# Kernel optimization log

Measured on AMD Instinct MI355X. Metric: run time of the kernel, lower is better.

The kernel has to match this reference:

```python
import jax, jax.numpy as jnp
import numpy as np

B, T, C, HS = 8, 2048, 1024, 64


def setup_inputs() -> dict:
    key = jax.random.key(0)
    ks = jax.random.split(key, 4)
    x = jax.random.normal(ks[0], (B, T, C), dtype=jnp.float32)
    Wq = jax.random.normal(ks[1], (C, HS), dtype=jnp.float32) * (C ** -0.5)
    Wk = jax.random.normal(ks[2], (C, HS), dtype=jnp.float32) * (C ** -0.5)
    Wv = jax.random.normal(ks[3], (C, HS), dtype=jnp.float32) * (C ** -0.5)
    mask = jnp.tril(jnp.ones((T, T), dtype=jnp.int32))  # causal mask
    return {"x": x, "mask": mask, "Wq": Wq, "Wk": Wk, "Wv": Wv}


def reference(x, mask, Wq, Wk, Wv):
    # x: [B,T,C]; bias-free projections to head_size
    q = jnp.einsum("btc,ch->bth", x, Wq)
    k = jnp.einsum("btc,ch->bth", x, Wk)
    v = jnp.einsum("btc,ch->bth", x, Wv)
    # NOTE: original scales by C**-0.5 (n_embd), not head_size**-0.5
    wei = jnp.einsum("bth,bsh->bts", q, k) * (x.shape[-1] ** -0.5)
    wei = jnp.where(mask[None, :, :] == 0, -jnp.inf, wei)
    wei = jax.nn.softmax(wei, axis=-1)
    # dropout is identity in eval / p=0
    out = jnp.einsum("bts,bsh->bth", wei, v)
    return out
```

## Files before the change

kernel.cpp:

```cpp
#include <hip/hip_runtime.h>
#include <hip/hip_bf16.h>


#define B_  8
#define T_  2048
#define C_  1024
#define HS_ 64
#define MROWS (B_ * T_)

typedef __attribute__((ext_vector_type(8))) short bf16x8;
typedef __attribute__((ext_vector_type(4))) float f32x4;
typedef __attribute__((ext_vector_type(4))) float float4v;

#define SCALE_LOG2 0.04508422037445829f

__device__ __forceinline__ short f2bs(float f) {
    __hip_bfloat16 h = __float2bfloat16(f);
    short s;
    __builtin_memcpy(&s, &h, 2);
    return s;
}

__global__ __launch_bounds__(256) void wt_kernel(
    const float* __restrict__ Wq,
    const float* __restrict__ Wk,
    const float* __restrict__ Wv,
    __hip_bfloat16* __restrict__ Wt) {
    __shared__ float tile[64][65];
    const int m  = blockIdx.x >> 4;
    const int r0 = (blockIdx.x & 15) * 64;
    const float* W = (m == 0) ? Wq : (m == 1) ? Wk : Wv;
    const int i = threadIdx.x >> 6;
    const int j = threadIdx.x & 63;
#pragma unroll
    for (int p = 0; p < 16; ++p) {
        int r = p * 4 + i;
        tile[r][j] = W[(size_t)(r0 + r) * HS_ + j];
    }
    __syncthreads();
#pragma unroll
    for (int p = 0; p < 16; ++p) {
        int h = p * 4 + i;
        Wt[(size_t)m * (HS_ * C_) + (size_t)h * C_ + r0 + j] =
            __float2bfloat16(tile[j][h]);
    }
}

__global__ __launch_bounds__(256, 2) void proj_kernel(
    const float* __restrict__ x,
    const __hip_bfloat16* __restrict__ Wt,
    __hip_bfloat16* __restrict__ Q,
    __hip_bfloat16* __restrict__ Kp,
    __hip_bfloat16* __restrict__ Vt)
{
    __shared__ float xtile[32 * 68];

    const int lane = threadIdx.x & 63;
    const int wave = threadIdx.x >> 6;
    const int quad = lane >> 4;
    const int l15  = lane & 15;
    const int row0 = blockIdx.x * 32;

    const float* gsrc[8];
#pragma unroll
    for (int rr = 0; rr < 8; ++rr)
        gsrc[rr] = x + (size_t)(row0 + wave * 8 + rr) * C_ + lane;

    const __hip_bfloat16* wbase[3];
#pragma unroll
    for (int j = 0; j < 3; ++j) {
        int nt = wave * 3 + j;
        int h  = ((nt & 3) * 16) + l15;
        wbase[j] = Wt + (size_t)(nt >> 2) * (HS_ * C_) + (size_t)h * C_ + quad * 8;
    }

    f32x4 acc[2][3];
#pragma unroll
    for (int rt = 0; rt < 2; ++rt)
#pragma unroll
        for (int j = 0; j < 3; ++j)
            acc[rt][j] = (f32x4){0.f, 0.f, 0.f, 0.f};

#pragma unroll 1
    for (int kc = 0; kc < C_; kc += 64) {
        if (kc) __syncthreads();

#pragma unroll
        for (int rr = 0; rr < 8; ++rr)
            __builtin_amdgcn_global_load_lds(
                (const __attribute__((address_space(1))) unsigned*)(gsrc[rr] + kc),
                (__attribute__((address_space(3))) unsigned*)
                    (&xtile[(wave * 8 + rr) * 68]),
                4, 0, 0);

        bf16x8 bfr[2][3];
#pragma unroll
        for (int ks = 0; ks < 2; ++ks)
#pragma unroll
            for (int j = 0; j < 3; ++j)
                bfr[ks][j] = *(const bf16x8*)(wbase[j] + kc + ks * 32);

        __syncthreads();

#pragma unroll
        for (int ks = 0; ks < 2; ++ks) {
            bf16x8 a[2];
#pragma unroll
            for (int rt = 0; rt < 2; ++rt) {
                const float4v* p = (const float4v*)
                    &xtile[(rt * 16 + l15) * 68 + ks * 32 + quad * 8];
                float4v f0 = p[0], f1 = p[1];
#pragma unroll
                for (int e = 0; e < 4; ++e) {
                    a[rt][e]     = f2bs(f0[e]);
                    a[rt][4 + e] = f2bs(f1[e]);
                }
            }
#pragma unroll
            for (int rt = 0; rt < 2; ++rt)
#pragma unroll
                for (int j = 0; j < 3; ++j)
                    acc[rt][j] = __builtin_amdgcn_mfma_f32_16x16x32_bf16(
                        a[rt], bfr[ks][j], acc[rt][j], 0, 0, 0);
        }
    }

#pragma unroll
    for (int rt = 0; rt < 2; ++rt) {
#pragma unroll
        for (int j = 0; j < 3; ++j) {
            int nt  = wave * 3 + j;
            int mtx = nt >> 2;
            int col = (nt & 3) * 16 + l15;
#pragma unroll
            for (int r = 0; r < 4; ++r) {
                int row = row0 + rt * 16 + quad * 4 + r;
                __hip_bfloat16 v = __float2bfloat16(acc[rt][j][r]);
                if (mtx == 0) {
                    Q[(size_t)row * HS_ + col] = v;
                } else if (mtx == 1) {
                    Kp[(size_t)row * HS_ + col] = v;
                } else {
                    int bidx = row >> 11;
                    int t    = row & 2047;
                    Vt[((size_t)bidx * HS_ + col) * T_ + t] = v;
                }
            }
        }
    }
}

__global__ __launch_bounds__(256) void attn_kernel(
    const __hip_bfloat16* __restrict__ Q,
    const __hip_bfloat16* __restrict__ Kp,
    const __hip_bfloat16* __restrict__ Vt,
    float* __restrict__ out)
{
    __shared__ __align__(16) __hip_bfloat16 plds[4][16 * 32];
    __shared__ float o_lds[4][16][64];
    __shared__ float l_lds[4][16][16];

    const int tid  = threadIdx.x;
    const int wv   = tid >> 6;
    const int lane = tid & 63;
    const int quad = lane >> 4;
    const int l15  = lane & 15;
    const int b    = blockIdx.x & 7;
    const int lt   = 127 - (blockIdx.x >> 3);
    const int qb   = lt * 16;
    const int rowg = b * T_ + qb;

    bf16x8 qf0 = *(const bf16x8*)(Q + (size_t)(rowg + l15) * HS_ + quad * 8);
    bf16x8 qf1 = *(const bf16x8*)(Q + (size_t)(rowg + l15) * HS_ + 32 + quad * 8);

    f32x4 o[4];
#pragma unroll
    for (int j = 0; j < 4; ++j) o[j] = (f32x4){0.f, 0.f, 0.f, 0.f};
    float lp[4] = {0.f, 0.f, 0.f, 0.f};

    __hip_bfloat16* pb = plds[wv];
    const int ntiles = qb / 32 + 1;

    auto load_kv = [&](int kb, bf16x8 kf[4], bf16x8 vf[4]) {
        const __hip_bfloat16* Kb = Kp + (size_t)(b * T_ + kb) * HS_;
        kf[0] = *(const bf16x8*)(Kb + (size_t)l15 * HS_ + quad * 8);
        kf[1] = *(const bf16x8*)(Kb + (size_t)l15 * HS_ + 32 + quad * 8);
        kf[2] = *(const bf16x8*)(Kb + (size_t)(16 + l15) * HS_ + quad * 8);
        kf[3] = *(const bf16x8*)(Kb + (size_t)(16 + l15) * HS_ + 32 + quad * 8);
#pragma unroll
        for (int j = 0; j < 4; ++j)
            vf[j] = *(const bf16x8*)
                (Vt + ((size_t)b * HS_ + j * 16 + l15) * T_ + kb + quad * 8);
    };

    bf16x8 kcur[4], vcur[4], knxt[4], vnxt[4];
    int t = wv;
    if (t < ntiles) load_kv(t * 32, kcur, vcur);

#pragma unroll 1
    for (; t < ntiles; t += 4) {
        const int tn = t + 4;
        load_kv(tn < ntiles ? tn * 32 : 0, knxt, vnxt);

        const int kb = t * 32;
        f32x4 s0 = (f32x4){0.f, 0.f, 0.f, 0.f};
        f32x4 s1 = (f32x4){0.f, 0.f, 0.f, 0.f};
        s0 = __builtin_amdgcn_mfma_f32_16x16x32_bf16(qf0, kcur[0], s0, 0, 0, 0);
        s0 = __builtin_amdgcn_mfma_f32_16x16x32_bf16(qf1, kcur[1], s0, 0, 0, 0);
        s1 = __builtin_amdgcn_mfma_f32_16x16x32_bf16(qf0, kcur[2], s1, 0, 0, 0);
        s1 = __builtin_amdgcn_mfma_f32_16x16x32_bf16(qf1, kcur[3], s1, 0, 0, 0);

        const bool diag = (kb + 31 > qb);
        float p0[4], p1[4];
#pragma unroll
        for (int r = 0; r < 4; ++r) {
            p0[r] = exp2f(s0[r] * SCALE_LOG2);
            p1[r] = exp2f(s1[r] * SCALE_LOG2);
            if (diag) {
                int row = qb + quad * 4 + r;
                if (kb + l15 > row)      p0[r] = 0.f;
                if (kb + 16 + l15 > row) p1[r] = 0.f;
            }
            lp[r] += p0[r] + p1[r];
        }

#pragma unroll
        for (int r = 0; r < 4; ++r) {
            pb[(quad * 4 + r) * 32 + l15]      = __float2bfloat16(p0[r]);
            pb[(quad * 4 + r) * 32 + 16 + l15] = __float2bfloat16(p1[r]);
        }
        asm volatile("s_waitcnt lgkmcnt(0)" ::: "memory");
        bf16x8 pf = *(const bf16x8*)(pb + l15 * 32 + quad * 8);

#pragma unroll
        for (int j = 0; j < 4; ++j)
            o[j] = __builtin_amdgcn_mfma_f32_16x16x32_bf16(pf, vcur[j], o[j], 0, 0, 0);

#pragma unroll
        for (int j = 0; j < 4; ++j) { kcur[j] = knxt[j]; vcur[j] = vnxt[j]; }
    }

#pragma unroll
    for (int j = 0; j < 4; ++j)
#pragma unroll
        for (int r = 0; r < 4; ++r)
            o_lds[wv][quad * 4 + r][j * 16 + l15] = o[j][r];
#pragma unroll
    for (int r = 0; r < 4; ++r)
        l_lds[wv][quad * 4 + r][l15] = lp[r];
    __syncthreads();

    if (tid < 16) {
        float s = 0.f;
#pragma unroll
        for (int w = 0; w < 4; ++w)
            for (int c = 0; c < 16; ++c) s += l_lds[w][tid][c];
        l_lds[0][tid][0] = s;
    }
    __syncthreads();

    const int h = tid & 63;
#pragma unroll
    for (int k = 0; k < 4; ++k) {
        int row = (tid >> 6) * 4 + k;
        float s = o_lds[0][row][h] + o_lds[1][row][h] +
                  o_lds[2][row][h] + o_lds[3][row][h];
        out[(size_t)(rowg + row) * HS_ + h] = s / l_lds[0][row][0];
    }
}

extern "C" void kernel_launch(void* const* d_in, const int* in_sizes, int n_in,
                              void* d_out, int out_size, void* d_ws, size_t ws_size,
                              hipStream_t stream) {
    (void)in_sizes; (void)n_in; (void)out_size; (void)ws_size;
    const float* x  = (const float*)d_in[0];
    const float* Wq = (const float*)d_in[2];
    const float* Wk = (const float*)d_in[3];
    const float* Wv = (const float*)d_in[4];

    __hip_bfloat16* ws = (__hip_bfloat16*)d_ws;
    __hip_bfloat16* Wt = ws;
    __hip_bfloat16* Q  = ws + 196608;
    __hip_bfloat16* Kp = ws + 196608 + 1048576;
    __hip_bfloat16* Vt = ws + 196608 + 2 * 1048576;

    wt_kernel<<<48, 256, 0, stream>>>(Wq, Wk, Wv, Wt);
    proj_kernel<<<MROWS / 32, 256, 0, stream>>>(x, Wt, Q, Kp, Vt);
    attn_kernel<<<(T_ / 16) * B_, 256, 0, stream>>>(Q, Kp, Vt, (float*)d_out);
}
```

Measured before the change: 169.8 us.

## Double-buffer projection loads and widen attention key tiles to 64

The projection kernel now double-buffers the x tile in LDS and the W fragments in registers. The next chunk's DMA and loads are issued before computing on the current one, removing a barrier per iteration. The attention kernel processes 64-key tiles per wave instead of 32 and drops the explicit register prefetch of the next tile. It also sets a 3-block occupancy hint, which trades cross-iteration prefetch for more work per iteration and more waves in flight.

```diff
diff --git a/kernel.cpp b/kernel.cpp
--- a/kernel.cpp
+++ b/kernel.cpp
@@ -53,7 +53,7 @@
     __hip_bfloat16* __restrict__ Kp,
     __hip_bfloat16* __restrict__ Vt)
 {
-    __shared__ float xtile[32 * 68];
+    __shared__ float xt[2][32 * 68];
 
     const int lane = threadIdx.x & 63;
     const int wave = threadIdx.x >> 6;
@@ -81,34 +81,48 @@
         for (int j = 0; j < 3; ++j)
             acc[rt][j] = (f32x4){0.f, 0.f, 0.f, 0.f};
 
+    bf16x8 bfr[2][2][3];
+
+#define ISSUE_DMA(buf, kc)                                                   \
+    do {                                                                     \
+        _Pragma("unroll")                                                    \
+        for (int rr = 0; rr < 8; ++rr)                                       \
+            __builtin_amdgcn_global_load_lds(                                \
+                (const __attribute__((address_space(1))) unsigned*)          \
+                    (gsrc[rr] + (kc)),                                       \
+                (__attribute__((address_space(3))) unsigned*)                \
+                    (&xt[buf][(wave * 8 + rr) * 68]),                        \
+                4, 0, 0);                                                    \
+    } while (0)
+
+#define LOAD_B(buf, kc)                                                      \
+    do {                                                                     \
+        _Pragma("unroll")                                                    \
+        for (int ks = 0; ks < 2; ++ks)                                       \
+            _Pragma("unroll")                                                \
+            for (int j = 0; j < 3; ++j)                                      \
+                bfr[buf][ks][j] =                                            \
+                    *(const bf16x8*)(wbase[j] + (kc) + ks * 32);             \
+    } while (0)
+
+    ISSUE_DMA(0, 0);
+    LOAD_B(0, 0);
+
+    int pb = 0;
 #pragma unroll 1
-    for (int kc = 0; kc < C_; kc += 64) {
-        if (kc) __syncthreads();
-
-#pragma unroll
-        for (int rr = 0; rr < 8; ++rr)
-            __builtin_amdgcn_global_load_lds(
-                (const __attribute__((address_space(1))) unsigned*)(gsrc[rr] + kc),
-                (__attribute__((address_space(3))) unsigned*)
-                    (&xtile[(wave * 8 + rr) * 68]),
-                4, 0, 0);
-
-        bf16x8 bfr[2][3];
-#pragma unroll
-        for (int ks = 0; ks < 2; ++ks)
-#pragma unroll
-            for (int j = 0; j < 3; ++j)
-                bfr[ks][j] = *(const bf16x8*)(wbase[j] + kc + ks * 32);
-
+    for (int kc = 0; kc < C_; kc += 64, pb ^= 1) {
         __syncthreads();
-
+        if (kc + 64 < C_) {
+            ISSUE_DMA(pb ^ 1, kc + 64);
+            LOAD_B(pb ^ 1, kc + 64);
+        }
 #pragma unroll
         for (int ks = 0; ks < 2; ++ks) {
             bf16x8 a[2];
 #pragma unroll
             for (int rt = 0; rt < 2; ++rt) {
                 const float4v* p = (const float4v*)
-                    &xtile[(rt * 16 + l15) * 68 + ks * 32 + quad * 8];
+                    &xt[pb][(rt * 16 + l15) * 68 + ks * 32 + quad * 8];
                 float4v f0 = p[0], f1 = p[1];
 #pragma unroll
                 for (int e = 0; e < 4; ++e) {
@@ -121,9 +135,11 @@
 #pragma unroll
                 for (int j = 0; j < 3; ++j)
                     acc[rt][j] = __builtin_amdgcn_mfma_f32_16x16x32_bf16(
-                        a[rt], bfr[ks][j], acc[rt][j], 0, 0, 0);
-        }
-    }
+                        a[rt], bfr[pb][ks][j], acc[rt][j], 0, 0, 0);
+        }
+    }
+#undef ISSUE_DMA
+#undef LOAD_B
 
 #pragma unroll
     for (int rt = 0; rt < 2; ++rt) {
@@ -150,13 +166,13 @@
     }
 }
 
-__global__ __launch_bounds__(256) void attn_kernel(
+__global__ __launch_bounds__(256, 3) void attn_kernel(
     const __hip_bfloat16* __restrict__ Q,
     const __hip_bfloat16* __restrict__ Kp,
     const __hip_bfloat16* __restrict__ Vt,
     float* __restrict__ out)
 {
-    __shared__ __align__(16) __hip_bfloat16 plds[4][16 * 32];
+    __shared__ __align__(16) __hip_bfloat16 plds[4][16 * 64];
     __shared__ float o_lds[4][16][64];
     __shared__ float l_lds[4][16][16];
 
@@ -179,65 +195,64 @@
     float lp[4] = {0.f, 0.f, 0.f, 0.f};
 
     __hip_bfloat16* pb = plds[wv];
-    const int ntiles = qb / 32 + 1;
-
-    auto load_kv = [&](int kb, bf16x8 kf[4], bf16x8 vf[4]) {
+    const int nt = (qb + 15) / 64 + 1;
+
+#pragma unroll 1
+    for (int t = wv; t < nt; t += 4) {
+        const int kb = t * 64;
         const __hip_bfloat16* Kb = Kp + (size_t)(b * T_ + kb) * HS_;
-        kf[0] = *(const bf16x8*)(Kb + (size_t)l15 * HS_ + quad * 8);
-        kf[1] = *(const bf16x8*)(Kb + (size_t)l15 * HS_ + 32 + quad * 8);
-        kf[2] = *(const bf16x8*)(Kb + (size_t)(16 + l15) * HS_ + quad * 8);
-        kf[3] = *(const bf16x8*)(Kb + (size_t)(16 + l15) * HS_ + 32 + quad * 8);
-#pragma unroll
-        for (int j = 0; j < 4; ++j)
-            vf[j] = *(const bf16x8*)
-                (Vt + ((size_t)b * HS_ + j * 16 + l15) * T_ + kb + quad * 8);
-    };
-
-    bf16x8 kcur[4], vcur[4], knxt[4], vnxt[4];
-    int t = wv;
-    if (t < ntiles) load_kv(t * 32, kcur, vcur);
-
-#pragma unroll 1
-    for (; t < ntiles; t += 4) {
-        const int tn = t + 4;
-        load_kv(tn < ntiles ? tn * 32 : 0, knxt, vnxt);
-
-        const int kb = t * 32;
-        f32x4 s0 = (f32x4){0.f, 0.f, 0.f, 0.f};
-        f32x4 s1 = (f32x4){0.f, 0.f, 0.f, 0.f};
-        s0 = __builtin_amdgcn_mfma_f32_16x16x32_bf16(qf0, kcur[0], s0, 0, 0, 0);
-        s0 = __builtin_amdgcn_mfma_f32_16x16x32_bf16(qf1, kcur[1], s0, 0, 0, 0);
-        s1 = __builtin_amdgcn_mfma_f32_16x16x32_bf16(qf0, kcur[2], s1, 0, 0, 0);
-        s1 = __builtin_amdgcn_mfma_f32_16x16x32_bf16(qf1, kcur[3], s1, 0, 0, 0);
-
-        const bool diag = (kb + 31 > qb);
-        float p0[4], p1[4];
-#pragma unroll
-        for (int r = 0; r < 4; ++r) {
-            p0[r] = exp2f(s0[r] * SCALE_LOG2);
-            p1[r] = exp2f(s1[r] * SCALE_LOG2);
-            if (diag) {
-                int row = qb + quad * 4 + r;
-                if (kb + l15 > row)      p0[r] = 0.f;
-                if (kb + 16 + l15 > row) p1[r] = 0.f;
+
+        bf16x8 kf[4][2];
+#pragma unroll
+        for (int c = 0; c < 4; ++c)
+#pragma unroll
+            for (int h = 0; h < 2; ++h)
+                kf[c][h] = *(const bf16x8*)
+                    (Kb + (size_t)(c * 16 + l15) * HS_ + h * 32 + quad * 8);
+        bf16x8 vf[2][4];
+#pragma unroll
+        for (int h = 0; h < 2; ++h)
+#pragma unroll
+            for (int j = 0; j < 4; ++j)
+                vf[h][j] = *(const bf16x8*)
+                    (Vt + ((size_t)b * HS_ + j * 16 + l15) * T_ + kb + h * 32 + quad * 8);
+
+        f32x4 s[4];
+#pragma unroll
+        for (int c = 0; c < 4; ++c) {
+            s[c] = (f32x4){0.f, 0.f, 0.f, 0.f};
+            s[c] = __builtin_amdgcn_mfma_f32_16x16x32_bf16(qf0, kf[c][0], s[c], 0, 0, 0);
+            s[c] = __builtin_amdgcn_mfma_f32_16x16x32_bf16(qf1, kf[c][1], s[c], 0, 0, 0);
+        }
+
+        const bool msk = (kb + 63 > qb);
+        float p[4][4];
+#pragma unroll
+        for (int c = 0; c < 4; ++c)
+#pragma unroll
+            for (int r = 0; r < 4; ++r) {
+                p[c][r] = exp2f(s[c][r] * SCALE_LOG2);
+                if (msk) {
+                    int row = qb + quad * 4 + r;
+                    if (kb + c * 16 + l15 > row) p[c][r] = 0.f;
+                }
+                lp[r] += p[c][r];
             }
-            lp[r] += p0[r] + p1[r];
-        }
-
-#pragma unroll
-        for (int r = 0; r < 4; ++r) {
-            pb[(quad * 4 + r) * 32 + l15]      = __float2bfloat16(p0[r]);
-            pb[(quad * 4 + r) * 32 + 16 + l15] = __float2bfloat16(p1[r]);
-        }
+
+#pragma unroll
+        for (int r = 0; r < 4; ++r)
+#pragma unroll
+            for (int c = 0; c < 4; ++c)
+                pb[(quad * 4 + r) * 64 + c * 16 + l15] = __float2bfloat16(p[c][r]);
         asm volatile("s_waitcnt lgkmcnt(0)" ::: "memory");
-        bf16x8 pf = *(const bf16x8*)(pb + l15 * 32 + quad * 8);
-
-#pragma unroll
-        for (int j = 0; j < 4; ++j)
-            o[j] = __builtin_amdgcn_mfma_f32_16x16x32_bf16(pf, vcur[j], o[j], 0, 0, 0);
-
-#pragma unroll
-        for (int j = 0; j < 4; ++j) { kcur[j] = knxt[j]; vcur[j] = vnxt[j]; }
+        bf16x8 pf0 = *(const bf16x8*)(pb + l15 * 64 + quad * 8);
+        bf16x8 pf1 = *(const bf16x8*)(pb + l15 * 64 + 32 + quad * 8);
+
+#pragma unroll
+        for (int j = 0; j < 4; ++j) {
+            o[j] = __builtin_amdgcn_mfma_f32_16x16x32_bf16(pf0, vf[0][j], o[j], 0, 0, 0);
+            o[j] = __builtin_amdgcn_mfma_f32_16x16x32_bf16(pf1, vf[1][j], o[j], 0, 0, 0);
+        }
     }
 
 #pragma unroll
```

Result: slower. 234.8 us (+38.3%).
